# Kernel tuning notes

Hardware: AMD Instinct MI355X
Metric: run time of the kernel (lower is better)

The kernel has to match this reference:

```python
import jax, jax.numpy as jnp
import numpy as np

TTL = 512   # total reviews per side (ragged across B examples)
B = 128     # batch of (user, item) pairs
PAD = 128   # padded review length
ASP = 8     # num aspects
D = 256     # feat_dim
BERT = 256  # bert hidden dim
NL = 4      # num_last_layers
NU = 10000
NI = 10000
EX_TEMP = 1.0  # ex_attn_temp


def setup_inputs() -> dict:
    key = jax.random.key(0)
    ks = jax.random.split(key, 32)
    def rn(i, shape, s=1.0):
        return jax.random.normal(ks[i], shape, dtype=jnp.float32) * s
    # sorted segment ids with every example owning >= 1 review
    u_seg = jnp.sort(jnp.concatenate([jnp.arange(B), jax.random.randint(ks[0], (TTL - B,), 0, B)]).astype(jnp.int32))
    i_seg = jnp.sort(jnp.concatenate([jnp.arange(B), jax.random.randint(ks[1], (TTL - B,), 0, B)]).astype(jnp.int32))
    return {
        "urevs_hidden": rn(2, (TTL, PAD, BERT * NL)),
        "irevs_hidden": rn(3, (TTL, PAD, BERT * NL)),
        "u_cls": rn(4, (TTL, BERT)),
        "i_cls": rn(5, (TTL, BERT)),
        "urevs_loc": jax.random.uniform(ks[6], (TTL, ASP, PAD), dtype=jnp.float32),
        "irevs_loc": jax.random.uniform(ks[7], (TTL, ASP, PAD), dtype=jnp.float32),
        "W_u_out": rn(8, (BERT * NL, D), 0.02), "b_u_out": rn(9, (D,), 0.02),
        "W_i_out": rn(10, (BERT * NL, D), 0.02), "b_i_out": rn(11, (D,), 0.02),
        "emb_aspect": rn(12, (ASP, D)),
        "w_ex_u": rn(13, (2 * D, 1), 0.02), "w_ex_i": rn(14, (2 * D, 1), 0.02),
        "w_im_u": rn(15, (2 * D, 1), 0.02), "w_im_i": rn(16, (2 * D, 1), 0.02),
        "W_ucls": rn(17, (BERT, D), 0.05), "W_icls": rn(18, (BERT, D), 0.05),
        "ex_W1": rn(19, (2 * D, D), 0.05), "ex_b1": rn(20, (D,), 0.05), "ex_W2": rn(21, (D, 1), 0.05),
        "im_W1": rn(22, (4 * D, D), 0.05), "im_b1": rn(23, (D,), 0.05), "im_W2": rn(24, (D, 1), 0.05),
        "bu_table": rn(25, (NU, 1)), "bt_table": rn(26, (NI, 1)),
        "gamma": rn(27, (ASP,)),
        "u_seg": u_seg, "i_seg": i_seg,
        "uid": jax.random.randint(ks[28], (B,), 0, NU, dtype=jnp.int32),
        "iid": jax.random.randint(ks[29], (B,), 0, NI, dtype=jnp.int32),
    }


def _seg_attn(scores, values, seg, nB):
    """Softmax over the ragged review axis (dim 0) within each segment, then weighted sum."""
    m = jax.ops.segment_max(scores, seg, num_segments=nB)
    e = jnp.exp(scores - m[seg])
    d = jax.ops.segment_sum(e, seg, num_segments=nB)
    return jax.ops.segment_sum((e / d[seg]) * values, seg, num_segments=nB)


def reference(urevs_hidden, irevs_hidden, u_cls, i_cls, urevs_loc, irevs_loc,
              W_u_out, b_u_out, W_i_out, b_i_out, emb_aspect,
              w_ex_u, w_ex_i, w_im_u, w_im_i, W_ucls, W_icls,
              ex_W1, ex_b1, ex_W2, im_W1, im_b1, im_W2,
              bu_table, bt_table, gamma, u_seg, i_seg, uid, iid):
    nB = uid.shape[0]

    def side(hidden, cls_tok, loc, W_out, b_out, w_ex, w_im, W_cls, seg):
        lang = hidden @ W_out + b_out                              # (R, P, D)
        asp = jnp.einsum('rap,rpd->rad', loc, lang)                # (R, A, D)
        asp_cat = jnp.concatenate(
            [asp, jnp.broadcast_to(emb_aspect, asp.shape)], axis=-1)
        sc_ex = jnp.tanh(asp_cat @ w_ex) / EX_TEMP                 # (R, A, 1)
        expl = _seg_attn(sc_ex, asp, seg, nB)                      # (B, A, D)
        cls_repr = cls_tok @ W_cls                                 # (R, D)
        avg = jnp.sum(lang, axis=1) / jnp.sum(lang != 0, axis=1)   # (R, D)
        cat = jnp.concatenate([cls_repr, avg], axis=-1)            # (R, 2D)
        sc_im = jnp.tanh(cat @ w_im)                               # (R, 1)
        impl = _seg_attn(sc_im, cat, seg, nB)                      # (B, 2D)
        return expl, impl

    u_expl, u_impl = side(urevs_hidden, u_cls, urevs_loc, W_u_out, b_u_out, w_ex_u, w_im_u, W_ucls, u_seg)
    i_expl, i_impl = side(irevs_hidden, i_cls, irevs_loc, W_i_out, b_i_out, w_ex_i, w_im_i, W_icls, i_seg)

    im_h = jax.nn.relu(jnp.concatenate([u_impl, i_impl], axis=-1) @ im_W1 + im_b1)
    pred = (bu_table[uid] + bt_table[iid] + im_h @ im_W2)[:, 0]    # (B,)
    ex_h = jax.nn.relu(jnp.concatenate([u_expl, i_expl], axis=-1) @ ex_W1 + ex_b1)
    ex_sc = (ex_h @ ex_W2)[..., 0]                                 # (B, A)
    return pred + ex_sc @ gamma
```

## Files before the change

### kernel.cpp

```cpp
#include <hip/hip_runtime.h>

#define TTL 512
#define NB  128
#define PAD 128
#define ASP 8
#define DD  256
#define HID 1024
#define ROWS9 (TTL * 9)

typedef float4 f4;

__device__ __forceinline__ float blockReduceSum(float v, float* red) {
    int t = threadIdx.x;
    red[t] = v;
    __syncthreads();
    #pragma unroll
    for (int s = 128; s > 0; s >>= 1) {
        if (t < s) red[t] += red[t + s];
        __syncthreads();
    }
    float r = red[0];
    __syncthreads();
    return r;
}

__global__ __launch_bounds__(256) void k_reduce(
    const float* __restrict__ uh, const float* __restrict__ ih,
    const float* __restrict__ uloc, const float* __restrict__ iloc,
    float* __restrict__ Hcat, float* __restrict__ Mult)
{
    const int r = blockIdx.x;
    const int side = blockIdx.y;
    const float* h   = side ? ih   : uh;
    const float* loc = side ? iloc : uloc;
    __shared__ float locT[PAD][ASP];
    const int t = threadIdx.x;

    for (int i = t; i < ASP * PAD; i += 256) {
        int a = i >> 7, p = i & 127;
        locT[p][a] = loc[r * ASP * PAD + i];
    }
    __syncthreads();

    float* mult = Mult + (size_t)side * ROWS9 + r * 9;
    if (t < ASP) {
        float s = 0.f;
        for (int p = 0; p < PAD; p++) s += locT[p][t];
        mult[t] = s;
    } else if (t == ASP) {
        mult[8] = 128.0f;
    }

    const f4* h4 = (const f4*)(h + (size_t)r * PAD * HID);
    f4 acc[9];
    #pragma unroll
    for (int a = 0; a < 9; a++) acc[a] = make_float4(0.f, 0.f, 0.f, 0.f);

    for (int p = 0; p < PAD; p++) {
        f4 v = h4[p * (HID / 4) + t];
        const f4* lrow = (const f4*)locT[p];
        f4 w0 = lrow[0], w1 = lrow[1];
        acc[8].x += v.x; acc[8].y += v.y; acc[8].z += v.z; acc[8].w += v.w;
        #define FMA_A(ai, ws) { acc[ai].x += (ws)*v.x; acc[ai].y += (ws)*v.y; \
                                acc[ai].z += (ws)*v.z; acc[ai].w += (ws)*v.w; }
        FMA_A(0, w0.x) FMA_A(1, w0.y) FMA_A(2, w0.z) FMA_A(3, w0.w)
        FMA_A(4, w1.x) FMA_A(5, w1.y) FMA_A(6, w1.z) FMA_A(7, w1.w)
        #undef FMA_A
    }

    f4* out = (f4*)(Hcat + ((size_t)side * ROWS9 + (size_t)r * 9) * HID);
    #pragma unroll
    for (int a = 0; a < 9; a++) out[a * (HID / 4) + t] = acc[a];
}

#define BM 64
#define BN 64
#define BKK 32
__global__ __launch_bounds__(256) void k_gemm(
    const float* __restrict__ A, const float* __restrict__ B,
    const float* __restrict__ bias, const float* __restrict__ mult,
    float* __restrict__ C, int M, int N, int K)
{
    __shared__ float As[BKK][BM];
    __shared__ float Bs[BKK][BN];
    const int t = threadIdx.x;
    const int m0 = blockIdx.x * BM, n0 = blockIdx.y * BN;
    const int tm = (t >> 4) << 2;
    const int tn = (t & 15) << 2;
    float c[4][4] = {};

    for (int k0 = 0; k0 < K; k0 += BKK) {
        #pragma unroll
        for (int i = 0; i < 2; i++) {
            int e = t + i * 256;
            int row = e >> 3;
            int kq = (e & 7) << 2;
            f4 v = *(const f4*)&A[(size_t)(m0 + row) * K + k0 + kq];
            As[kq + 0][row] = v.x; As[kq + 1][row] = v.y;
            As[kq + 2][row] = v.z; As[kq + 3][row] = v.w;
        }
        #pragma unroll
        for (int i = 0; i < 2; i++) {
            int e = t + i * 256;
            int row = e >> 4;
            int dq = (e & 15) << 2;
            *(f4*)&Bs[row][dq] = *(const f4*)&B[(size_t)(k0 + row) * N + n0 + dq];
        }
        __syncthreads();
        #pragma unroll
        for (int k = 0; k < BKK; k++) {
            f4 a4 = *(const f4*)&As[k][tm];
            f4 b4 = *(const f4*)&Bs[k][tn];
            c[0][0] += a4.x * b4.x; c[0][1] += a4.x * b4.y; c[0][2] += a4.x * b4.z; c[0][3] += a4.x * b4.w;
            c[1][0] += a4.y * b4.x; c[1][1] += a4.y * b4.y; c[1][2] += a4.y * b4.z; c[1][3] += a4.y * b4.w;
            c[2][0] += a4.z * b4.x; c[2][1] += a4.z * b4.y; c[2][2] += a4.z * b4.z; c[2][3] += a4.z * b4.w;
            c[3][0] += a4.w * b4.x; c[3][1] += a4.w * b4.y; c[3][2] += a4.w * b4.z; c[3][3] += a4.w * b4.w;
        }
        __syncthreads();
    }

    #pragma unroll
    for (int i = 0; i < 4; i++) {
        int m = m0 + tm + i;
        f4 v = make_float4(c[i][0], c[i][1], c[i][2], c[i][3]);
        if (mult) {
            float mm = mult[m];
            v.x += mm * bias[n0 + tn + 0];
            v.y += mm * bias[n0 + tn + 1];
            v.z += mm * bias[n0 + tn + 2];
            v.w += mm * bias[n0 + tn + 3];
        }
        *(f4*)&C[(size_t)m * N + n0 + tn] = v;
    }
}

__global__ __launch_bounds__(256) void k_ea(
    const float* __restrict__ emb, const float* __restrict__ wexu,
    const float* __restrict__ wexi, float* __restrict__ ea)
{
    int a = blockIdx.x, side = blockIdx.y;
    const float* w = (side ? wexi : wexu) + DD;
    __shared__ float red[256];
    float v = emb[a * DD + threadIdx.x] * w[threadIdx.x];
    float s = blockReduceSum(v, red);
    if (threadIdx.x == 0) ea[side * ASP + a] = s;
}

__global__ __launch_bounds__(256) void k_scores(
    const float* __restrict__ AspAvg, const float* __restrict__ ClsRepr,
    const float* __restrict__ wexu, const float* __restrict__ wexi,
    const float* __restrict__ wimu, const float* __restrict__ wimi,
    const float* __restrict__ ea,
    float* __restrict__ sc_ex, float* __restrict__ sc_im)
{
    const int r = blockIdx.x, side = blockIdx.y, t = threadIdx.x;
    const float* wex = side ? wexi : wexu;
    const float* wim = side ? wimi : wimu;
    const float* rowbase = AspAvg + ((size_t)side * ROWS9 + (size_t)r * 9) * DD;
    __shared__ float red[256];
    for (int a = 0; a < 8; a++) {
        float v = rowbase[a * DD + t] * wex[t];
        float s = blockReduceSum(v, red);
        if (t == 0) sc_ex[(side * TTL + r) * ASP + a] = tanhf(s + ea[side * ASP + a]);
    }
    float v = ClsRepr[((size_t)side * TTL + r) * DD + t] * wim[t]
            + (rowbase[8 * DD + t] * (1.0f / 128.0f)) * wim[DD + t];
    float s = blockReduceSum(v, red);
    if (t == 0) sc_im[side * TTL + r] = tanhf(s);
}

__global__ __launch_bounds__(256) void k_segattn(
    const float* __restrict__ AspAvg, const float* __restrict__ ClsRepr,
    const float* __restrict__ sc_ex, const float* __restrict__ sc_im,
    const int* __restrict__ useg, const int* __restrict__ iseg,
    float* __restrict__ Expl, float* __restrict__ Impl)
{
    const int b = blockIdx.x, side = blockIdx.y, t = threadIdx.x;
    const int* seg = side ? iseg : useg;
    int lo = 0, hi = TTL;
    while (lo < hi) { int mid = (lo + hi) >> 1; if (seg[mid] < b) lo = mid + 1; else hi = mid; }
    const int start = lo;
    hi = TTL;
    while (lo < hi) { int mid = (lo + hi) >> 1; if (seg[mid] <= b) lo = mid + 1; else hi = mid; }
    const int end = lo;

    const float* scx = sc_ex + side * TTL * ASP;
    for (int a = 0; a < 8; a++) {
        float m = -1e30f;
        for (int r = start; r < end; r++) m = fmaxf(m, scx[r * ASP + a]);
        float den = 0.f;
        for (int r = start; r < end; r++) den += expf(scx[r * ASP + a] - m);
        float acc = 0.f;
        for (int r = start; r < end; r++) {
            float w = expf(scx[r * ASP + a] - m) / den;
            acc += w * AspAvg[((size_t)side * ROWS9 + (size_t)r * 9 + a) * DD + t];
        }
        Expl[(((size_t)side * NB + b) * ASP + a) * DD + t] = acc;
    }
    {
        const float* sci = sc_im + side * TTL;
        float m = -1e30f;
        for (int r = start; r < end; r++) m = fmaxf(m, sci[r]);
        float den = 0.f;
        for (int r = start; r < end; r++) den += expf(sci[r] - m);
        float a1 = 0.f, a2 = 0.f;
        for (int r = start; r < end; r++) {
            float w = expf(sci[r] - m) / den;
            a1 += w * ClsRepr[((size_t)side * TTL + r) * DD + t];
            a2 += w * (AspAvg[((size_t)side * ROWS9 + (size_t)r * 9 + 8) * DD + t] * (1.0f / 128.0f));
        }
        Impl[((size_t)side * NB + b) * (2 * DD) + t] = a1;
        Impl[((size_t)side * NB + b) * (2 * DD) + DD + t] = a2;
    }
}

__global__ __launch_bounds__(256) void k_final(
    const float* __restrict__ Expl, const float* __restrict__ Impl,
    const float* __restrict__ imW1, const float* __restrict__ imb1, const float* __restrict__ imW2,
    const float* __restrict__ exW1, const float* __restrict__ exb1, const float* __restrict__ exW2,
    const float* __restrict__ bu, const float* __restrict__ bt, const float* __restrict__ gamma,
    const int* __restrict__ uid, const int* __restrict__ iid, float* __restrict__ out)
{
    const int b = blockIdx.x, t = threadIdx.x;
    __shared__ float catIm[4 * DD];
    __shared__ float catEx[2 * DD][ASP];
    __shared__ float red[256];

    catIm[t]       = Impl[(size_t)b * 512 + t];
    catIm[t + 256] = Impl[(size_t)b * 512 + t + 256];
    catIm[t + 512] = Impl[((size_t)NB + b) * 512 + t];
    catIm[t + 768] = Impl[((size_t)NB + b) * 512 + t + 256];
    #pragma unroll
    for (int a = 0; a < 8; a++) {
        catEx[t][a]       = Expl[((size_t)b * ASP + a) * DD + t];
        catEx[t + 256][a] = Expl[(((size_t)NB + b) * ASP + a) * DD + t];
    }
    __syncthreads();

    float g[8];
    #pragma unroll
    for (int a = 0; a < 8; a++) g[a] = gamma[a];

    float acc = imb1[t];
    for (int k = 0; k < 1024; k++) acc += catIm[k] * imW1[k * DD + t];
    float imh = fmaxf(acc, 0.f);
    float part = imh * imW2[t];

    float ex[8];
    #pragma unroll
    for (int a = 0; a < 8; a++) ex[a] = exb1[t];
    for (int k = 0; k < 512; k++) {
        float w = exW1[k * DD + t];
        #pragma unroll
        for (int a = 0; a < 8; a++) ex[a] += catEx[k][a] * w;
    }
    float exs = 0.f;
    #pragma unroll
    for (int a = 0; a < 8; a++) exs += fmaxf(ex[a], 0.f) * g[a];
    part += exs * exW2[t];

    float tot = blockReduceSum(part, red);
    if (t == 0) out[b] = bu[uid[b]] + bt[iid[b]] + tot;
}

extern "C" void kernel_launch(void* const* d_in, const int* in_sizes, int n_in,
                              void* d_out, int out_size, void* d_ws, size_t ws_size,
                              hipStream_t stream) {
    const float* uh    = (const float*)d_in[0];
    const float* ih    = (const float*)d_in[1];
    const float* ucls  = (const float*)d_in[2];
    const float* icls  = (const float*)d_in[3];
    const float* uloc  = (const float*)d_in[4];
    const float* iloc  = (const float*)d_in[5];
    const float* Wuo   = (const float*)d_in[6];
    const float* buo   = (const float*)d_in[7];
    const float* Wio   = (const float*)d_in[8];
    const float* bio   = (const float*)d_in[9];
    const float* emb   = (const float*)d_in[10];
    const float* wexu  = (const float*)d_in[11];
    const float* wexi  = (const float*)d_in[12];
    const float* wimu  = (const float*)d_in[13];
    const float* wimi  = (const float*)d_in[14];
    const float* Wucls = (const float*)d_in[15];
    const float* Wicls = (const float*)d_in[16];
    const float* exW1  = (const float*)d_in[17];
    const float* exb1  = (const float*)d_in[18];
    const float* exW2  = (const float*)d_in[19];
    const float* imW1  = (const float*)d_in[20];
    const float* imb1  = (const float*)d_in[21];
    const float* imW2  = (const float*)d_in[22];
    const float* bu    = (const float*)d_in[23];
    const float* bt    = (const float*)d_in[24];
    const float* gam   = (const float*)d_in[25];
    const int*   useg  = (const int*)d_in[26];
    const int*   iseg  = (const int*)d_in[27];
    const int*   uid   = (const int*)d_in[28];
    const int*   iid   = (const int*)d_in[29];
    float* out = (float*)d_out;

    char* w = (char*)d_ws;
    auto carve = [&](size_t bytes) { void* p = (void*)w; w += (bytes + 255) & ~(size_t)255; return p; };
    float* Hcat    = (float*)carve(2ULL * ROWS9 * HID * 4);
    float* Mult    = (float*)carve(2ULL * ROWS9 * 4);
    float* AspAvg  = (float*)carve(2ULL * ROWS9 * DD * 4);
    float* ClsRepr = (float*)carve(2ULL * TTL * DD * 4);
    float* sc_ex   = (float*)carve(2ULL * TTL * ASP * 4);
    float* sc_im   = (float*)carve(2ULL * TTL * 4);
    float* ea      = (float*)carve(2ULL * ASP * 4);
    float* Expl    = (float*)carve(2ULL * NB * ASP * DD * 4);
    float* Impl    = (float*)carve(2ULL * NB * 2 * DD * 4);
    (void)ws_size; (void)n_in; (void)in_sizes; (void)out_size;

    k_reduce<<<dim3(TTL, 2), 256, 0, stream>>>(uh, ih, uloc, iloc, Hcat, Mult);

    for (int s = 0; s < 2; s++) {
        k_gemm<<<dim3(ROWS9 / BM, DD / BN), 256, 0, stream>>>(
            Hcat + (size_t)s * ROWS9 * HID, s ? Wio : Wuo, s ? bio : buo,
            Mult + (size_t)s * ROWS9, AspAvg + (size_t)s * ROWS9 * DD,
            ROWS9, DD, HID);
    }
    for (int s = 0; s < 2; s++) {
        k_gemm<<<dim3(TTL / BM, DD / BN), 256, 0, stream>>>(
            s ? icls : ucls, s ? Wicls : Wucls, nullptr, nullptr,
            ClsRepr + (size_t)s * TTL * DD, TTL, DD, DD);
    }

    k_ea<<<dim3(ASP, 2), 256, 0, stream>>>(emb, wexu, wexi, ea);
    k_scores<<<dim3(TTL, 2), 256, 0, stream>>>(AspAvg, ClsRepr, wexu, wexi, wimu, wimi, ea, sc_ex, sc_im);
    k_segattn<<<dim3(NB, 2), 256, 0, stream>>>(AspAvg, ClsRepr, sc_ex, sc_im, useg, iseg, Expl, Impl);
    k_final<<<dim3(NB), 256, 0, stream>>>(Expl, Impl, imW1, imb1, imW2,
                                          exW1, exb1, exW2, bu, bt, gam, uid, iid, out);
}
```

Baseline: 867.5 us.

## Prefetch reduce loads, split-K merged GEMM, wave-shuffle scores, per-aspect segattn

The reduce kernel now software-prefetches the next four hidden rows into registers so loads overlap the FMAs. The two per-side projection GEMMs are merged into one launch with a split-K of 2 writing partial sums, and a separate kernel adds the partials plus the scaled bias. The scores kernel replaces nine serialized shared-memory tree reductions with wavefront shuffles and a single barrier. Segment attention gains a grid dimension over aspects for more parallel blocks. In exchange there is extra partial-buffer traffic and one more launch.

```diff
diff --git a/kernel.cpp b/kernel.cpp
--- a/kernel.cpp
+++ b/kernel.cpp
@@ -7,6 +7,8 @@
 #define DD  256
 #define HID 1024
 #define ROWS9 (TTL * 9)
+#define MTOT (2 * ROWS9)
+#define KS 2
 
 typedef float4 f4;
 
@@ -51,21 +53,35 @@
         mult[8] = 128.0f;
     }
 
-    const f4* h4 = (const f4*)(h + (size_t)r * PAD * HID);
+    const f4* h4 = (const f4*)(h + (size_t)r * PAD * HID) + t;
     f4 acc[9];
     #pragma unroll
     for (int a = 0; a < 9; a++) acc[a] = make_float4(0.f, 0.f, 0.f, 0.f);
 
-    for (int p = 0; p < PAD; p++) {
-        f4 v = h4[p * (HID / 4) + t];
-        const f4* lrow = (const f4*)locT[p];
-        f4 w0 = lrow[0], w1 = lrow[1];
-        acc[8].x += v.x; acc[8].y += v.y; acc[8].z += v.z; acc[8].w += v.w;
-        #define FMA_A(ai, ws) { acc[ai].x += (ws)*v.x; acc[ai].y += (ws)*v.y; \
-                                acc[ai].z += (ws)*v.z; acc[ai].w += (ws)*v.w; }
-        FMA_A(0, w0.x) FMA_A(1, w0.y) FMA_A(2, w0.z) FMA_A(3, w0.w)
-        FMA_A(4, w1.x) FMA_A(5, w1.y) FMA_A(6, w1.z) FMA_A(7, w1.w)
-        #undef FMA_A
+    f4 buf[4];
+    #pragma unroll
+    for (int j = 0; j < 4; j++) buf[j] = h4[j * (HID / 4)];
+
+    for (int p = 0; p < PAD; p += 4) {
+        f4 nxt[4];
+        if (p + 4 < PAD) {
+            #pragma unroll
+            for (int j = 0; j < 4; j++) nxt[j] = h4[(p + 4 + j) * (HID / 4)];
+        }
+        #pragma unroll
+        for (int j = 0; j < 4; j++) {
+            const f4* lrow = (const f4*)locT[p + j];
+            f4 w0 = lrow[0], w1 = lrow[1];
+            f4 v = buf[j];
+            acc[8].x += v.x; acc[8].y += v.y; acc[8].z += v.z; acc[8].w += v.w;
+            #define FMA_A(ai, ws) { acc[ai].x += (ws)*v.x; acc[ai].y += (ws)*v.y; \
+                                    acc[ai].z += (ws)*v.z; acc[ai].w += (ws)*v.w; }
+            FMA_A(0, w0.x) FMA_A(1, w0.y) FMA_A(2, w0.z) FMA_A(3, w0.w)
+            FMA_A(4, w1.x) FMA_A(5, w1.y) FMA_A(6, w1.z) FMA_A(7, w1.w)
+            #undef FMA_A
+        }
+        #pragma unroll
+        for (int j = 0; j < 4; j++) buf[j] = nxt[j];
     }
 
     f4* out = (f4*)(Hcat + ((size_t)side * ROWS9 + (size_t)r * 9) * HID);
@@ -76,9 +92,86 @@
 #define BM 64
 #define BN 64
 #define BKK 32
+__global__ __launch_bounds__(256) void k_gemm2(
+    const float* __restrict__ A, const float* __restrict__ Bu, const float* __restrict__ Bi,
+    float* __restrict__ Part)
+{
+    __shared__ float As[BKK][BM];
+    __shared__ float Bs[BKK][BN];
+    const int t = threadIdx.x;
+    const int m0 = blockIdx.x * BM, n0 = blockIdx.y * BN;
+    const int side = (m0 >= ROWS9) ? 1 : 0;
+    const float* B = side ? Bi : Bu;
+    const int kbeg = blockIdx.z * (HID / KS);
+    const int kend = kbeg + (HID / KS);
+    const int tm = (t >> 4) << 2;
+    const int tn = (t & 15) << 2;
+    float c[4][4] = {};
+
+    for (int k0 = kbeg; k0 < kend; k0 += BKK) {
+        #pragma unroll
+        for (int i = 0; i < 2; i++) {
+            int e = t + i * 256;
+            int row = e >> 3;
+            int kq = (e & 7) << 2;
+            f4 v = *(const f4*)&A[(size_t)(m0 + row) * HID + k0 + kq];
+            As[kq + 0][row] = v.x; As[kq + 1][row] = v.y;
+            As[kq + 2][row] = v.z; As[kq + 3][row] = v.w;
+        }
+        #pragma unroll
+        for (int i = 0; i < 2; i++) {
+            int e = t + i * 256;
+            int row = e >> 4;
+            int dq = (e & 15) << 2;
+            *(f4*)&Bs[row][dq] = *(const f4*)&B[(size_t)(k0 + row) * DD + n0 + dq];
+        }
+        __syncthreads();
+        #pragma unroll
+        for (int k = 0; k < BKK; k++) {
+            f4 a4 = *(const f4*)&As[k][tm];
+            f4 b4 = *(const f4*)&Bs[k][tn];
+            c[0][0] += a4.x * b4.x; c[0][1] += a4.x * b4.y; c[0][2] += a4.x * b4.z; c[0][3] += a4.x * b4.w;
+            c[1][0] += a4.y * b4.x; c[1][1] += a4.y * b4.y; c[1][2] += a4.y * b4.z; c[1][3] += a4.y * b4.w;
+            c[2][0] += a4.z * b4.x; c[2][1] += a4.z * b4.y; c[2][2] += a4.z * b4.z; c[2][3] += a4.z * b4.w;
+            c[3][0] += a4.w * b4.x; c[3][1] += a4.w * b4.y; c[3][2] += a4.w * b4.z; c[3][3] += a4.w * b4.w;
+        }
+        __syncthreads();
+    }
+
+    float* P = Part + (size_t)blockIdx.z * MTOT * DD;
+    #pragma unroll
+    for (int i = 0; i < 4; i++) {
+        *(f4*)&P[(size_t)(m0 + tm + i) * DD + n0 + tn] =
+            make_float4(c[i][0], c[i][1], c[i][2], c[i][3]);
+    }
+}
+
+__global__ __launch_bounds__(256) void k_gfin(
+    const float* __restrict__ Part, const float* __restrict__ Mult,
+    const float* __restrict__ bu_bias, const float* __restrict__ bi_bias,
+    float* __restrict__ C)
+{
+    const size_t idx = (size_t)blockIdx.x * 256 + threadIdx.x;
+    const f4* P4 = (const f4*)Part;
+    f4 v = P4[idx];
+    #pragma unroll
+    for (int z = 1; z < KS; z++) {
+        f4 w = P4[idx + (size_t)z * (MTOT * DD / 4)];
+        v.x += w.x; v.y += w.y; v.z += w.z; v.w += w.w;
+    }
+    const int m = (int)(idx >> 6);
+    const int n = ((int)idx & 63) << 2;
+    const float* bias = (m >= ROWS9) ? bi_bias : bu_bias;
+    float mm = Mult[m];
+    v.x += mm * bias[n + 0];
+    v.y += mm * bias[n + 1];
+    v.z += mm * bias[n + 2];
+    v.w += mm * bias[n + 3];
+    ((f4*)C)[idx] = v;
+}
+
 __global__ __launch_bounds__(256) void k_gemm(
     const float* __restrict__ A, const float* __restrict__ B,
-    const float* __restrict__ bias, const float* __restrict__ mult,
     float* __restrict__ C, int M, int N, int K)
 {
     __shared__ float As[BKK][BM];
@@ -121,16 +214,8 @@
 
     #pragma unroll
     for (int i = 0; i < 4; i++) {
-        int m = m0 + tm + i;
-        f4 v = make_float4(c[i][0], c[i][1], c[i][2], c[i][3]);
-        if (mult) {
-            float mm = mult[m];
-            v.x += mm * bias[n0 + tn + 0];
-            v.y += mm * bias[n0 + tn + 1];
-            v.z += mm * bias[n0 + tn + 2];
-            v.w += mm * bias[n0 + tn + 3];
-        }
-        *(f4*)&C[(size_t)m * N + n0 + tn] = v;
+        *(f4*)&C[(size_t)(m0 + tm + i) * N + n0 + tn] =
+            make_float4(c[i][0], c[i][1], c[i][2], c[i][3]);
     }
 }
 
@@ -157,16 +242,31 @@
     const float* wex = side ? wexi : wexu;
     const float* wim = side ? wimi : wimu;
     const float* rowbase = AspAvg + ((size_t)side * ROWS9 + (size_t)r * 9) * DD;
-    __shared__ float red[256];
-    for (int a = 0; a < 8; a++) {
-        float v = rowbase[a * DD + t] * wex[t];
-        float s = blockReduceSum(v, red);
-        if (t == 0) sc_ex[(side * TTL + r) * ASP + a] = tanhf(s + ea[side * ASP + a]);
-    }
-    float v = ClsRepr[((size_t)side * TTL + r) * DD + t] * wim[t]
-            + (rowbase[8 * DD + t] * (1.0f / 128.0f)) * wim[DD + t];
-    float s = blockReduceSum(v, red);
-    if (t == 0) sc_im[side * TTL + r] = tanhf(s);
+    __shared__ float sums[4][9];
+
+    float wx = wex[t];
+    float v[9];
+    #pragma unroll
+    for (int a = 0; a < 8; a++) v[a] = rowbase[a * DD + t] * wx;
+    v[8] = ClsRepr[((size_t)side * TTL + r) * DD + t] * wim[t]
+         + (rowbase[8 * DD + t] * (1.0f / 128.0f)) * wim[DD + t];
+
+    #pragma unroll
+    for (int off = 32; off > 0; off >>= 1) {
+        #pragma unroll
+        for (int a = 0; a < 9; a++) v[a] += __shfl_down(v[a], off, 64);
+    }
+    if ((t & 63) == 0) {
+        int wv = t >> 6;
+        #pragma unroll
+        for (int a = 0; a < 9; a++) sums[wv][a] = v[a];
+    }
+    __syncthreads();
+    if (t < 9) {
+        float s = sums[0][t] + sums[1][t] + sums[2][t] + sums[3][t];
+        if (t < 8) sc_ex[(side * TTL + r) * ASP + t] = tanhf(s + ea[side * ASP + t]);
+        else       sc_im[side * TTL + r] = tanhf(s);
+    }
 }
 
 __global__ __launch_bounds__(256) void k_segattn(
@@ -175,7 +275,7 @@
     const int* __restrict__ useg, const int* __restrict__ iseg,
     float* __restrict__ Expl, float* __restrict__ Impl)
 {
-    const int b = blockIdx.x, side = blockIdx.y, t = threadIdx.x;
+    const int b = blockIdx.x, side = blockIdx.y, a = blockIdx.z, t = threadIdx.x;
     const int* seg = side ? iseg : useg;
     int lo = 0, hi = TTL;
     while (lo < hi) { int mid = (lo + hi) >> 1; if (seg[mid] < b) lo = mid + 1; else hi = mid; }
@@ -184,8 +284,8 @@
     while (lo < hi) { int mid = (lo + hi) >> 1; if (seg[mid] <= b) lo = mid + 1; else hi = mid; }
     const int end = lo;
 
-    const float* scx = sc_ex + side * TTL * ASP;
-    for (int a = 0; a < 8; a++) {
+    if (a < 8) {
+        const float* scx = sc_ex + side * TTL * ASP;
         float m = -1e30f;
         for (int r = start; r < end; r++) m = fmaxf(m, scx[r * ASP + a]);
         float den = 0.f;
@@ -196,8 +296,7 @@
             acc += w * AspAvg[((size_t)side * ROWS9 + (size_t)r * 9 + a) * DD + t];
         }
         Expl[(((size_t)side * NB + b) * ASP + a) * DD + t] = acc;
-    }
-    {
+    } else {
         const float* sci = sc_im + side * TTL;
         float m = -1e30f;
         for (int r = start; r < end; r++) m = fmaxf(m, sci[r]);
@@ -302,6 +401,7 @@
     auto carve = [&](size_t bytes) { void* p = (void*)w; w += (bytes + 255) & ~(size_t)255; return p; };
     float* Hcat    = (float*)carve(2ULL * ROWS9 * HID * 4);
     float* Mult    = (float*)carve(2ULL * ROWS9 * 4);
+    float* Part    = (float*)carve((size_t)KS * MTOT * DD * 4);
     float* AspAvg  = (float*)carve(2ULL * ROWS9 * DD * 4);
     float* ClsRepr = (float*)carve(2ULL * TTL * DD * 4);
     float* sc_ex   = (float*)carve(2ULL * TTL * ASP * 4);
@@ -313,21 +413,18 @@
 
     k_reduce<<<dim3(TTL, 2), 256, 0, stream>>>(uh, ih, uloc, iloc, Hcat, Mult);
 
-    for (int s = 0; s < 2; s++) {
-        k_gemm<<<dim3(ROWS9 / BM, DD / BN), 256, 0, stream>>>(
-            Hcat + (size_t)s * ROWS9 * HID, s ? Wio : Wuo, s ? bio : buo,
-            Mult + (size_t)s * ROWS9, AspAvg + (size_t)s * ROWS9 * DD,
-            ROWS9, DD, HID);
-    }
+    k_gemm2<<<dim3(MTOT / BM, DD / BN, KS), 256, 0, stream>>>(Hcat, Wuo, Wio, Part);
+    k_gfin<<<dim3(MTOT * DD / 4 / 256), 256, 0, stream>>>(Part, Mult, buo, bio, AspAvg);
+
     for (int s = 0; s < 2; s++) {
         k_gemm<<<dim3(TTL / BM, DD / BN), 256, 0, stream>>>(
-            s ? icls : ucls, s ? Wicls : Wucls, nullptr, nullptr,
+            s ? icls : ucls, s ? Wicls : Wucls,
             ClsRepr + (size_t)s * TTL * DD, TTL, DD, DD);
     }
 
     k_ea<<<dim3(ASP, 2), 256, 0, stream>>>(emb, wexu, wexi, ea);
     k_scores<<<dim3(TTL, 2), 256, 0, stream>>>(AspAvg, ClsRepr, wexu, wexi, wimu, wimi, ea, sc_ex, sc_im);
-    k_segattn<<<dim3(NB, 2), 256, 0, stream>>>(AspAvg, ClsRepr, sc_ex, sc_im, useg, iseg, Expl, Impl);
+    k_segattn<<<dim3(NB, 2, 9), 256, 0, stream>>>(AspAvg, ClsRepr, sc_ex, sc_im, useg, iseg, Expl, Impl);
     k_final<<<dim3(NB), 256, 0, stream>>>(Expl, Impl, imW1, imb1, imW2,
                                           exW1, exb1, exW2, bu, bt, gam, uid, iid, out);
 }
```

Measured after the change: 776.6 us. 1.12x faster.
